# Optimization experiments

Hardware: AMD Instinct MI355X
Metric: run time of the kernel (lower is better)

Reference implementation:

```python
import jax, jax.numpy as jnp
import numpy as np

OUTPUT_SIZE = 16384          # number of map units (must be a perfect square)
SIDE = 128.0                 # sqrt(OUTPUT_SIZE)
SIGMA = 2.0                  # neighbourhood std-dev (non-trainable weight in original)
B, D = 2048, 256


def setup_inputs() -> dict:
    key = jax.random.key(0)
    k1, k2 = jax.random.split(key)
    x = jax.random.normal(k1, (B, D), dtype=jnp.float32)
    kernel = jax.random.normal(k2, (D, OUTPUT_SIZE), dtype=jnp.float32) * 0.1
    return {"x": x, "kernel": kernel}


def _grid_coords():
    # 2D coordinates of each flattened map unit: unit k -> (k // side, k % side)
    idx = jnp.arange(OUTPUT_SIZE, dtype=jnp.float32)
    return jnp.floor(idx / SIDE), jnp.mod(idx, SIDE)  # each (size,)


def reference(x, kernel):
    # Squared Euclidean distance of every sample to every prototype: (B, size).
    # Same math as tf.norm(x[:, :, None] - kernel[None])**2, expressed as a GEMM.
    norms2 = (jnp.sum(x * x, axis=1, keepdims=True)
              - 2.0 * (x @ kernel)
              + jnp.sum(kernel * kernel, axis=0, keepdims=True))
    norms2 = jnp.maximum(norms2, 0.0)

    # Winner-take-all unit per sample, mapped to 2D grid coordinates.
    wta = jnp.argmin(norms2, axis=1).astype(jnp.float32)        # (B,)
    mean_r = jnp.floor(wta / SIDE)                               # (B,)
    mean_c = jnp.mod(wta, SIDE)                                  # (B,)

    # Gaussian neighbourhood over the 2D grid, flattened: (B, size).
    gr, gc = _grid_coords()
    dr = gr[None, :] - mean_r[:, None]
    dc = gc[None, :] - mean_c[:, None]
    radials = jnp.exp(-0.5 / (SIGMA * SIGMA) * (dr * dr + dc * dc))

    return radials * norms2
```

## Files before the change

kernel.cpp:

```cpp
#include <hip/hip_runtime.h>
#include <hip/hip_fp16.h>

#define OUTN 16384
#define BATCH 2048
#define DIM   256

typedef _Float16 half8 __attribute__((ext_vector_type(8)));
typedef float    floatx4 __attribute__((ext_vector_type(4)));
typedef unsigned long long u64;

__device__ __forceinline__ void gl2lds16(const void* g, void* l) {
    __builtin_amdgcn_global_load_lds(
        (const __attribute__((address_space(1))) void*)g,
        (__attribute__((address_space(3))) void*)l, 16, 0, 0);
}

__device__ __forceinline__ u64 packkey(float v, int col) {
    unsigned u = __float_as_uint(v);
    u = (u & 0x80000000u) ? ~u : (u | 0x80000000u);
    return ((u64)u << 32) | (unsigned)col;
}
__device__ __forceinline__ float unpackval(u64 p) {
    unsigned u = (unsigned)(p >> 32);
    u = (u & 0x80000000u) ? (u & 0x7fffffffu) : ~u;
    return __uint_as_float(u);
}

__global__ __launch_bounds__(256) void prep_all(
        const float* __restrict__ x, const float* __restrict__ kern,
        _Float16* __restrict__ xh, float* __restrict__ rown,
        _Float16* __restrict__ kT, float* __restrict__ colnp) {
    int blk = blockIdx.x, t = threadIdx.x;
    if (blk < 512) {
        __shared__ float tile[64][65];
        __shared__ float npart[4][64];
        int tx = t & 63, ty = t >> 6;
        int j0 = (blk >> 1) * 64;
        int dhalf = blk & 1, dbase = dhalf * 128;
        float nrm = 0.f;
        for (int pc = 0; pc < 2; pc++) {
            int dc = dbase + pc * 64;
            __syncthreads();
            for (int it = 0; it < 16; it++) {
                int d = dc + ty + it * 4;
                float v = kern[(size_t)d * OUTN + j0 + tx];
                tile[ty + it * 4][tx] = v;
                nrm = fmaf(v, v, nrm);
            }
            __syncthreads();
            for (int c = t; c < 512; c += 256) {
                int j = c >> 3, o8 = (c & 7) * 8;
                half8 h;
                for (int u = 0; u < 8; u++) h[u] = (_Float16)tile[o8 + u][j];
                *(half8*)&kT[(size_t)(j0 + j) * DIM + dc + o8] = h;
            }
        }
        npart[ty][tx] = nrm;
        __syncthreads();
        if (t < 64)
            colnp[(size_t)dhalf * OUTN + j0 + t] =
                npart[0][t] + npart[1][t] + npart[2][t] + npart[3][t];
    } else {
        int b = blk - 512;
        float v = x[b * DIM + t];
        xh[b * DIM + t] = (_Float16)v;
        float s = v * v;
        for (int off = 32; off; off >>= 1) s += __shfl_down(s, off, 64);
        __shared__ float wsum[4];
        if ((t & 63) == 0) wsum[t >> 6] = s;
        __syncthreads();
        if (t == 0) rown[b] = wsum[0] + wsum[1] + wsum[2] + wsum[3];
    }
}

template <bool NF16>
__global__ __launch_bounds__(256) void gemm_norms(
        const _Float16* __restrict__ xh, const _Float16* __restrict__ kT,
        const float* __restrict__ rown, const float* __restrict__ colnp,
        void* __restrict__ n2out, u64* __restrict__ blockcand) {
    __shared__ __align__(16) char smem[32768];
    _Float16* As = (_Float16*)smem;
    _Float16* Bs = (_Float16*)(smem + 16384);
    u64* cand = (u64*)smem;
    int tid  = threadIdx.x;
    int col0 = blockIdx.x * 128;
    int row0 = blockIdx.y * 128;
    int wid = tid >> 6, lane = tid & 63;
    int wr = wid >> 1, wc = wid & 1;
    int l15 = lane & 15, l4 = lane >> 4;
    int xh7 = l15 & 7;

    floatx4 acc[4][4];
    for (int i = 0; i < 4; i++)
        for (int j = 0; j < 4; j++)
            acc[i][j] = (floatx4){0.f, 0.f, 0.f, 0.f};

    for (int kt = 0; kt < 4; kt++) {
        int k0 = kt * 64;
        for (int it = 0; it < 4; it++) {
            int chunk = it * 256 + tid;
            int r = chunk >> 3, gg = chunk & 7;
            int ksw = (gg ^ (r & 7)) * 8;
            gl2lds16(&xh[(size_t)(row0 + r) * DIM + k0 + ksw], &As[chunk * 8]);
            gl2lds16(&kT[(size_t)(col0 + r) * DIM + k0 + ksw], &Bs[chunk * 8]);
        }
        __syncthreads();
        for (int s = 0; s < 2; s++) {
            int g = s * 4 + l4;
            int sw = (g ^ xh7) * 8;
            half8 af[4], bf[4];
            for (int i = 0; i < 4; i++)
                af[i] = *(half8*)&As[(wr * 64 + i * 16 + l15) * 64 + sw];
            for (int j = 0; j < 4; j++)
                bf[j] = *(half8*)&Bs[(wc * 64 + j * 16 + l15) * 64 + sw];
            for (int i = 0; i < 4; i++)
                for (int j = 0; j < 4; j++)
                    acc[i][j] = __builtin_amdgcn_mfma_f32_16x16x32_f16(
                        af[i], bf[j], acc[i][j], 0, 0, 0);
        }
        __syncthreads();
    }

    float cn[4]; int oc[4];
    for (int j = 0; j < 4; j++) {
        oc[j] = col0 + wc * 64 + j * 16 + l15;
        cn[j] = colnp[oc[j]] + colnp[OUTN + oc[j]];
    }
    for (int i = 0; i < 4; i++) {
        for (int r = 0; r < 4; r++) {
            int row_l = wr * 64 + i * 16 + l4 * 4 + r;
            int orow  = row0 + row_l;
            float rn = rown[orow];
            u64 best = ~0ull;
            for (int j = 0; j < 4; j++) {
                float val = rn + cn[j] - 2.0f * acc[i][j][r];
                size_t oi = (size_t)orow * OUTN + oc[j];
                if (NF16) ((_Float16*)n2out)[oi] = (_Float16)val;
                else      ((float*)n2out)[oi]    = val;
                u64 p = packkey(val, oc[j]);
                if (p < best) best = p;
            }
            cand[row_l * 32 + wc * 16 + l15] = best;
        }
    }
    __syncthreads();
    if (tid < 128) {
        u64 m1 = ~0ull, m2 = ~0ull;
        for (int s = 0; s < 32; s++) {
            u64 v = cand[tid * 32 + s];
            if (v < m1) { m2 = m1; m1 = v; }
            else if (v < m2) { m2 = v; }
        }
        size_t base = (size_t)(row0 + tid) * 256 + blockIdx.x * 2;
        blockcand[base]     = m1;
        blockcand[base + 1] = m2;
    }
}

template <bool NF16>
__global__ __launch_bounds__(256) void refine_finalize(
        const u64* __restrict__ blockcand, const float* __restrict__ x,
        const float* __restrict__ kern, const float* __restrict__ colnp,
        const void* __restrict__ n2in, float* __restrict__ out) {
    int b = blockIdx.x, t = threadIdx.x;
    __shared__ float xrow[DIM];
    __shared__ u64 red[256];
    xrow[t] = x[b * DIM + t];
    u64 e = blockcand[(size_t)b * 256 + t];
    red[t] = e;
    __syncthreads();
    for (int off = 128; off; off >>= 1) {
        if (t < off) { u64 o = red[t + off]; if (o < red[t]) red[t] = o; }
        __syncthreads();
    }
    float minv = unpackval(red[0]);
    __syncthreads();

    float ve = unpackval(e);
    u64 p = ~0ull;
    if (ve <= minv + 0.125f) {
        int j = (int)(e & 0xffffffffu);
        float dot = 0.f;
        for (int d = 0; d < DIM; d++)
            dot = fmaf(xrow[d], kern[(size_t)d * OUTN + j], dot);
        p = packkey((colnp[j] + colnp[OUTN + j]) - 2.0f * dot, j);
    }
    red[t] = p;
    __syncthreads();
    for (int off = 128; off; off >>= 1) {
        if (t < off) { u64 o = red[t + off]; if (o < red[t]) red[t] = o; }
        __syncthreads();
    }
    int w = (int)(red[0] & 0xffffffffu);
    int wrr = w >> 7, wcc = w & 127;

    const _Float16* r16 = (const _Float16*)n2in + (size_t)b * OUTN;
    const float*    r32 = (const float*)n2in    + (size_t)b * OUTN;
    float* rowp = out + (size_t)b * OUTN;
    for (int it = 0; it < 16; it++) {
        int idx4 = it * 256 + t;
        int j0 = idx4 * 4;
        int r  = j0 >> 7, c0 = j0 & 127;
        int dr = r - wrr, drsq = dr * dr;
        float4 res;
        {
            int dc = c0 - wcc;     int d2 = drsq + dc * dc;
            float v = (d2 <= 720) ? (NF16 ? (float)r16[j0]     : r32[j0])     : 0.f;
            res.x = (d2 <= 720) ? __expf(-0.125f * (float)d2) * fmaxf(v, 0.f) : 0.f;
        }
        {
            int dc = c0 + 1 - wcc; int d2 = drsq + dc * dc;
            float v = (d2 <= 720) ? (NF16 ? (float)r16[j0 + 1] : r32[j0 + 1]) : 0.f;
            res.y = (d2 <= 720) ? __expf(-0.125f * (float)d2) * fmaxf(v, 0.f) : 0.f;
        }
        {
            int dc = c0 + 2 - wcc; int d2 = drsq + dc * dc;
            float v = (d2 <= 720) ? (NF16 ? (float)r16[j0 + 2] : r32[j0 + 2]) : 0.f;
            res.z = (d2 <= 720) ? __expf(-0.125f * (float)d2) * fmaxf(v, 0.f) : 0.f;
        }
        {
            int dc = c0 + 3 - wcc; int d2 = drsq + dc * dc;
            float v = (d2 <= 720) ? (NF16 ? (float)r16[j0 + 3] : r32[j0 + 3]) : 0.f;
            res.w = (d2 <= 720) ? __expf(-0.125f * (float)d2) * fmaxf(v, 0.f) : 0.f;
        }
        ((float4*)rowp)[idx4] = res;
    }
}

extern "C" void kernel_launch(void* const* d_in, const int* in_sizes, int n_in,
                              void* d_out, int out_size, void* d_ws, size_t ws_size,
                              hipStream_t stream) {
    const float* x    = (const float*)d_in[0];
    const float* kern = (const float*)d_in[1];
    float* out = (float*)d_out;
    char* ws = (char*)d_ws;

    _Float16* xh   = (_Float16*)(ws);
    _Float16* kT   = (_Float16*)(ws + (1u << 20));
    float*   colnp = (float*)(ws + (9u << 20));
    float*   rown  = (float*)(ws + (9u << 20) + (128u << 10));
    u64* blockcand = (u64*)(ws + (10u << 20));
    void*    n2h   = (void*)(ws + (14u << 20));
    bool f16path = ws_size >= ((size_t)78 << 20);

    prep_all<<<2560, 256, 0, stream>>>(x, kern, xh, rown, kT, colnp);
    if (f16path) {
        gemm_norms<true><<<dim3(OUTN / 128, BATCH / 128), 256, 0, stream>>>(
            xh, kT, rown, colnp, n2h, blockcand);
        refine_finalize<true><<<BATCH, 256, 0, stream>>>(
            blockcand, x, kern, colnp, n2h, out);
    } else {
        gemm_norms<false><<<dim3(OUTN / 128, BATCH / 128), 256, 0, stream>>>(
            xh, kT, rown, colnp, (void*)out, blockcand);
        refine_finalize<false><<<BATCH, 256, 0, stream>>>(
            blockcand, x, kern, colnp, (const void*)out, out);
    }
}
```

Before: 202.7 us.

## Add fp32 transposed kernel copy for refine, swizzle candidate LDS, separable gaussian

The prep kernel now also writes a row-major fp32 transposed copy of the kernel when the workspace is large enough. The refine dot product then reads contiguous float4 values instead of a 256-element column gathered with a 64KB stride. The candidate buffer in the GEMM epilogue is XOR-swizzled to avoid LDS bank conflicts. The finalize loop factors the gaussian into row and column exponentials, skips whole float4 groups outside the radius, and uses vector loads of the norms. The cost is 16MB of extra fp32 writes in prep, which may offset part of the gain, plus a dependence on workspace size.

```diff
diff --git a/kernel.cpp b/kernel.cpp
--- a/kernel.cpp
+++ b/kernel.cpp
@@ -6,6 +6,7 @@
 #define DIM   256
 
 typedef _Float16 half8 __attribute__((ext_vector_type(8)));
+typedef _Float16 half4 __attribute__((ext_vector_type(4)));
 typedef float    floatx4 __attribute__((ext_vector_type(4)));
 typedef unsigned long long u64;
 
@@ -29,7 +30,8 @@
 __global__ __launch_bounds__(256) void prep_all(
         const float* __restrict__ x, const float* __restrict__ kern,
         _Float16* __restrict__ xh, float* __restrict__ rown,
-        _Float16* __restrict__ kT, float* __restrict__ colnp) {
+        _Float16* __restrict__ kT, float* __restrict__ colnp,
+        float* __restrict__ kT32) {
     int blk = blockIdx.x, t = threadIdx.x;
     if (blk < 512) {
         __shared__ float tile[64][65];
@@ -54,6 +56,14 @@
                 for (int u = 0; u < 8; u++) h[u] = (_Float16)tile[o8 + u][j];
                 *(half8*)&kT[(size_t)(j0 + j) * DIM + dc + o8] = h;
             }
+            if (kT32) {
+                for (int c = t; c < 1024; c += 256) {
+                    int j = c >> 4, o4 = (c & 15) * 4;
+                    float4 f = make_float4(tile[o4][j], tile[o4 + 1][j],
+                                           tile[o4 + 2][j], tile[o4 + 3][j]);
+                    *(float4*)&kT32[(size_t)(j0 + j) * DIM + dc + o4] = f;
+                }
+            }
         }
         npart[ty][tx] = nrm;
         __syncthreads();
@@ -122,6 +132,7 @@
     }
 
     float cn[4]; int oc[4];
+    int cid = wc * 16 + l15;
     for (int j = 0; j < 4; j++) {
         oc[j] = col0 + wc * 64 + j * 16 + l15;
         cn[j] = colnp[oc[j]] + colnp[OUTN + oc[j]];
@@ -140,14 +151,14 @@
                 u64 p = packkey(val, oc[j]);
                 if (p < best) best = p;
             }
-            cand[row_l * 32 + wc * 16 + l15] = best;
+            cand[row_l * 32 + (cid ^ (row_l & 31))] = best;
         }
     }
     __syncthreads();
     if (tid < 128) {
         u64 m1 = ~0ull, m2 = ~0ull;
         for (int s = 0; s < 32; s++) {
-            u64 v = cand[tid * 32 + s];
+            u64 v = cand[tid * 32 + (s ^ (tid & 31))];
             if (v < m1) { m2 = m1; m1 = v; }
             else if (v < m2) { m2 = v; }
         }
@@ -157,11 +168,12 @@
     }
 }
 
-template <bool NF16>
+template <bool NF16, bool KT32P>
 __global__ __launch_bounds__(256) void refine_finalize(
         const u64* __restrict__ blockcand, const float* __restrict__ x,
         const float* __restrict__ kern, const float* __restrict__ colnp,
-        const void* __restrict__ n2in, float* __restrict__ out) {
+        const float* __restrict__ kT32, const void* __restrict__ n2in,
+        float* __restrict__ out) {
     int b = blockIdx.x, t = threadIdx.x;
     __shared__ float xrow[DIM];
     __shared__ u64 red[256];
@@ -181,8 +193,19 @@
     if (ve <= minv + 0.125f) {
         int j = (int)(e & 0xffffffffu);
         float dot = 0.f;
-        for (int d = 0; d < DIM; d++)
-            dot = fmaf(xrow[d], kern[(size_t)d * OUTN + j], dot);
+        if (KT32P) {
+            const float4* kc = (const float4*)&kT32[(size_t)j * DIM];
+            for (int d4 = 0; d4 < DIM / 4; d4++) {
+                float4 kv = kc[d4];
+                dot = fmaf(xrow[d4 * 4 + 0], kv.x, dot);
+                dot = fmaf(xrow[d4 * 4 + 1], kv.y, dot);
+                dot = fmaf(xrow[d4 * 4 + 2], kv.z, dot);
+                dot = fmaf(xrow[d4 * 4 + 3], kv.w, dot);
+            }
+        } else {
+            for (int d = 0; d < DIM; d++)
+                dot = fmaf(xrow[d], kern[(size_t)d * OUTN + j], dot);
+        }
         p = packkey((colnp[j] + colnp[OUTN + j]) - 2.0f * dot, j);
     }
     red[t] = p;
@@ -197,31 +220,34 @@
     const _Float16* r16 = (const _Float16*)n2in + (size_t)b * OUTN;
     const float*    r32 = (const float*)n2in    + (size_t)b * OUTN;
     float* rowp = out + (size_t)b * OUTN;
+
+    int c0 = (t & 31) * 4, rb = t >> 5;
+    int dc0 = c0 - wcc;
+    int q0 = dc0 * dc0, q1 = (dc0 + 1) * (dc0 + 1),
+        q2 = (dc0 + 2) * (dc0 + 2), q3 = (dc0 + 3) * (dc0 + 3);
+    int qmin = min(min(q0, q1), min(q2, q3));
+    float ec0 = __expf(-0.125f * (float)q0), ec1 = __expf(-0.125f * (float)q1),
+          ec2 = __expf(-0.125f * (float)q2), ec3 = __expf(-0.125f * (float)q3);
+
     for (int it = 0; it < 16; it++) {
         int idx4 = it * 256 + t;
-        int j0 = idx4 * 4;
-        int r  = j0 >> 7, c0 = j0 & 127;
+        int r = it * 8 + rb;
         int dr = r - wrr, drsq = dr * dr;
-        float4 res;
-        {
-            int dc = c0 - wcc;     int d2 = drsq + dc * dc;
-            float v = (d2 <= 720) ? (NF16 ? (float)r16[j0]     : r32[j0])     : 0.f;
-            res.x = (d2 <= 720) ? __expf(-0.125f * (float)d2) * fmaxf(v, 0.f) : 0.f;
-        }
-        {
-            int dc = c0 + 1 - wcc; int d2 = drsq + dc * dc;
-            float v = (d2 <= 720) ? (NF16 ? (float)r16[j0 + 1] : r32[j0 + 1]) : 0.f;
-            res.y = (d2 <= 720) ? __expf(-0.125f * (float)d2) * fmaxf(v, 0.f) : 0.f;
-        }
-        {
-            int dc = c0 + 2 - wcc; int d2 = drsq + dc * dc;
-            float v = (d2 <= 720) ? (NF16 ? (float)r16[j0 + 2] : r32[j0 + 2]) : 0.f;
-            res.z = (d2 <= 720) ? __expf(-0.125f * (float)d2) * fmaxf(v, 0.f) : 0.f;
-        }
-        {
-            int dc = c0 + 3 - wcc; int d2 = drsq + dc * dc;
-            float v = (d2 <= 720) ? (NF16 ? (float)r16[j0 + 3] : r32[j0 + 3]) : 0.f;
-            res.w = (d2 <= 720) ? __expf(-0.125f * (float)d2) * fmaxf(v, 0.f) : 0.f;
+        float4 res = make_float4(0.f, 0.f, 0.f, 0.f);
+        if (drsq + qmin <= 720) {
+            float va, vb, vc, vd;
+            if (NF16) {
+                half4 h = *(const half4*)&r16[idx4 * 4];
+                va = (float)h[0]; vb = (float)h[1]; vc = (float)h[2]; vd = (float)h[3];
+            } else {
+                float4 f = ((const float4*)r32)[idx4];
+                va = f.x; vb = f.y; vc = f.z; vd = f.w;
+            }
+            float er = __expf(-0.125f * (float)drsq);
+            if (drsq + q0 <= 720) res.x = er * ec0 * fmaxf(va, 0.f);
+            if (drsq + q1 <= 720) res.y = er * ec1 * fmaxf(vb, 0.f);
+            if (drsq + q2 <= 720) res.z = er * ec2 * fmaxf(vc, 0.f);
+            if (drsq + q3 <= 720) res.w = er * ec3 * fmaxf(vd, 0.f);
         }
         ((float4*)rowp)[idx4] = res;
     }
@@ -241,18 +267,24 @@
     float*   rown  = (float*)(ws + (9u << 20) + (128u << 10));
     u64* blockcand = (u64*)(ws + (10u << 20));
     void*    n2h   = (void*)(ws + (14u << 20));
-    bool f16path = ws_size >= ((size_t)78 << 20);
-
-    prep_all<<<2560, 256, 0, stream>>>(x, kern, xh, rown, kT, colnp);
+    bool f16path  = ws_size >= ((size_t)78 << 20);
+    bool kt32path = ws_size >= ((size_t)94 << 20);
+    float* kT32 = kt32path ? (float*)(ws + (78u << 20)) : nullptr;
+
+    prep_all<<<2560, 256, 0, stream>>>(x, kern, xh, rown, kT, colnp, kT32);
     if (f16path) {
         gemm_norms<true><<<dim3(OUTN / 128, BATCH / 128), 256, 0, stream>>>(
             xh, kT, rown, colnp, n2h, blockcand);
-        refine_finalize<true><<<BATCH, 256, 0, stream>>>(
-            blockcand, x, kern, colnp, n2h, out);
+        if (kt32path)
+            refine_finalize<true, true><<<BATCH, 256, 0, stream>>>(
+                blockcand, x, kern, colnp, kT32, n2h, out);
+        else
+            refine_finalize<true, false><<<BATCH, 256, 0, stream>>>(
+                blockcand, x, kern, colnp, nullptr, n2h, out);
     } else {
         gemm_norms<false><<<dim3(OUTN / 128, BATCH / 128), 256, 0, stream>>>(
             xh, kT, rown, colnp, (void*)out, blockcand);
-        refine_finalize<false><<<BATCH, 256, 0, stream>>>(
-            blockcand, x, kern, colnp, (const void*)out, out);
-    }
-}
+        refine_finalize<false, false><<<BATCH, 256, 0, stream>>>(
+            blockcand, x, kern, colnp, nullptr, (const void*)out, out);
+    }
+}
```

New measurement: 200.2 us. No clear change (-1.2%).
